# Optimization experiments

Hardware: AMD Instinct MI355X
Metric: run time of the kernel (lower is better)

## Reference

```python
import jax, jax.numpy as jnp
import numpy as np

N = 10000          # in_size: number of nodes
H = 8              # n_heads
D = 64             # dimension per head
FEAT = H * D       # 512, node feature width (heads concatenated)
N_NETS = 3         # number of input networks (modalities)
E = 160000         # edges per network


def setup_inputs() -> dict:
    key = jax.random.key(0)
    ks = jax.random.split(key, 6)
    x = jax.random.normal(ks[0], (N, FEAT), dtype=jnp.float32)
    # n_id: global node ids in the sampled data_flow (here: full graph, identity)
    n_id = jnp.arange(N, dtype=jnp.int32)
    # per-network GAT attention values (non-negative, like softmaxed attn)
    attns = jax.random.uniform(ks[1], (N_NETS, E, H), dtype=jnp.float32)
    # per-network global edge indices (row 0 = source, row 1 = target)
    edges_global = jax.random.randint(ks[2], (N_NETS, 2, E), 0, N, dtype=jnp.int32)
    # learned per-head, per-network combination weights: net_weights[:, net_idx]
    net_weights = jax.random.uniform(ks[3], (H, N_NETS), dtype=jnp.float32)
    # ComboWGATConv linear: in = dimension*n_heads, out = dimension per head (concat)
    W = jax.random.normal(ks[4], (FEAT, FEAT), dtype=jnp.float32) * 0.02
    bias = jnp.zeros((FEAT,), dtype=jnp.float32)
    return {"x": x, "n_id": n_id, "attns": attns, "edges_global": edges_global,
            "net_weights": net_weights, "W": W, "bias": bias}


def reference(x, n_id, attns, edges_global, net_weights, W, bias):
    n_nodes, feat = x.shape
    n_nets, e, h = attns.shape
    d = feat // h

    # --- multi-network attention combination (aggregat_edge_weights) ---
    # w_cogat_attn[i] = net_weights[:, i] * attns[i]   -> (nets, E, H)
    w_attn = attns * net_weights.T[:, None, :]
    # Sparse add/coalesce across modalities: since the subsequent scatter-sum is
    # linear in edge weights, summing duplicate edges is equivalent to keeping
    # the concatenated (non-coalesced) edge list. nets-major flatten order.
    agg_alpha = w_attn.reshape(n_nets * e, h)                      # (Etot, H)
    agg_edges = edges_global.transpose(1, 0, 2).reshape(2, n_nets * e)  # (2, Etot)

    # --- edge_idx_from_global_to_local: invert n_id lookup ---
    inv = jnp.zeros((N,), dtype=jnp.int32).at[n_id].set(
        jnp.arange(n_nodes, dtype=jnp.int32))
    src = inv[agg_edges[0]]
    dst = inv[agg_edges[1]]

    # --- ComboWGATConv with externally supplied alpha (layer_no == 0) ---
    x_l = x[n_id]                                   # gather subgraph features
    hfeat = (x_l @ W).reshape(n_nodes, h, d)        # per-head transform
    msg = agg_alpha[:, :, None] * hfeat[src]        # (Etot, H, D) gather+weight
    out = jax.ops.segment_sum(msg, dst, num_segments=n_nodes)  # scatter-sum
    out = out.reshape(n_nodes, feat) + bias         # concat heads + bias
    return out
```

## Files before the change

### kernel.cpp

```cpp
#include <hip/hip_runtime.h>

#define NNODES 10000
#define NHEADS 8
#define DHEAD 64
#define FEAT 512
#define NNETS 3
#define EDGES 160000
#define ETOT (NNETS * EDGES)
#define NBUCK 4
#define BUCKSZ 2500
#define NKEY (NNODES * NBUCK)

#define CVTX_BLKS 5000
#define CVTW_BLKS 256
#define HIST_BLKS 1875
#define INV_BLKS 40
#define SCAT_BLKS 1875
#define GEMM_BLKS 316

typedef unsigned short ushort_t;
typedef __bf16 bf16x8 __attribute__((ext_vector_type(8)));
typedef float f32x4 __attribute__((ext_vector_type(4)));
typedef unsigned u32x4 __attribute__((ext_vector_type(4)));

static __device__ __forceinline__ ushort_t f2b(float f) {
    unsigned u = __float_as_uint(f);
    unsigned r = u + 0x7FFF + ((u >> 16) & 1);
    return (ushort_t)(r >> 16);
}

static __device__ __forceinline__ void mfma16(f32x4& d, bf16x8 a, bf16x8 b) {
    asm volatile("v_mfma_f32_16x16x32_bf16 %0, %1, %2, %0" : "+v"(d) : "v"(a), "v"(b));
}

#define GLDS(gp, lp)                                                                     \
    __builtin_amdgcn_global_load_lds((const __attribute__((address_space(1))) void*)(gp), \
                                     (__attribute__((address_space(3))) void*)(lp), 16, 0, 0)

__global__ __launch_bounds__(256) void prep_fused_kernel(
    const float* __restrict__ x, ushort_t* __restrict__ xb, const float* __restrict__ W,
    ushort_t* __restrict__ wbt, const int* __restrict__ edges, int* __restrict__ counts,
    const int* __restrict__ n_id, int* __restrict__ inv) {
    __shared__ float tile[32][33];
    int b = blockIdx.x;
    int t = threadIdx.x;
    if (b < CVTX_BLKS) {
        int i = (b * 256 + t) * 4;
        float4 v = *(const float4*)(x + i);
        ushort4 o;
        o.x = f2b(v.x);
        o.y = f2b(v.y);
        o.z = f2b(v.z);
        o.w = f2b(v.w);
        *(ushort4*)(xb + i) = o;
    } else if (b < CVTX_BLKS + CVTW_BLKS) {
        int bb = b - CVTX_BLKS;
        int n0 = (bb & 15) * 32, k0 = (bb >> 4) * 32;
        int r = t >> 3, c4 = (t & 7) * 4;
        float4 v = *(const float4*)(&W[(size_t)(k0 + r) * FEAT + n0 + c4]);
        tile[r][c4 + 0] = v.x;
        tile[r][c4 + 1] = v.y;
        tile[r][c4 + 2] = v.z;
        tile[r][c4 + 3] = v.w;
        __syncthreads();
        ushort4 o;
        o.x = f2b(tile[c4 + 0][r]);
        o.y = f2b(tile[c4 + 1][r]);
        o.z = f2b(tile[c4 + 2][r]);
        o.w = f2b(tile[c4 + 3][r]);
        int ncol = n0 + r;
        int nperm = (ncol & 63) * 8 + (ncol >> 6);
        *(ushort4*)(&wbt[(size_t)nperm * FEAT + k0 + c4]) = o;
    } else if (b < CVTX_BLKS + CVTW_BLKS + HIST_BLKS) {
        int eid = (b - CVTX_BLKS - CVTW_BLKS) * 256 + t;
        int net = eid / EDGES;
        int e = eid - net * EDGES;
        int srcg = edges[net * (2 * EDGES) + e];
        int dstg = edges[net * (2 * EDGES) + EDGES + e];
        atomicAdd(&counts[dstg * NBUCK + srcg / BUCKSZ], 1);
    } else {
        int i = (b - CVTX_BLKS - CVTW_BLKS - HIST_BLKS) * 256 + t;
        if (i < NNODES) inv[n_id[i]] = i;
    }
}

__global__ __launch_bounds__(1024) void scan_kernel(const int* __restrict__ counts,
                                                    int* __restrict__ offsets) {
    __shared__ int wincl[16];
    int t = threadIdx.x;
    int ln = t & 63;
    int w = t >> 6;
    int4 v[10];
    int mysum = 0;
    if (t < 1000) {
        const int4* cp = (const int4*)(counts + t * 40);
#pragma unroll
        for (int i = 0; i < 10; ++i) {
            v[i] = cp[i];
            mysum += v[i].x + v[i].y + v[i].z + v[i].w;
        }
    }
    int s = mysum;
#pragma unroll
    for (int o = 1; o < 64; o <<= 1) {
        int u = __shfl_up(s, o, 64);
        if (ln >= o) s += u;
    }
    if (ln == 63) wincl[w] = s;
    __syncthreads();
    if (w == 0) {
        int ws = (ln < 16) ? wincl[ln] : 0;
#pragma unroll
        for (int o = 1; o < 16; o <<= 1) {
            int u = __shfl_up(ws, o, 64);
            if (ln >= o) ws += u;
        }
        if (ln < 16) wincl[ln] = ws;
    }
    __syncthreads();
    int base = ((w > 0) ? wincl[w - 1] : 0) + s - mysum;
    if (t < 1000) {
        int running = base;
        int* op = offsets + t * 40;
#pragma unroll
        for (int i = 0; i < 10; ++i) {
            op[i * 4 + 0] = running; running += v[i].x;
            op[i * 4 + 1] = running; running += v[i].y;
            op[i * 4 + 2] = running; running += v[i].z;
            op[i * 4 + 3] = running; running += v[i].w;
        }
        if (t == 999) offsets[NKEY] = running;
    }
}

__global__ __launch_bounds__(256) void gemm_scatter_kernel(
    const ushort_t* __restrict__ xb, const ushort_t* __restrict__ wbt,
    ushort_t* __restrict__ Cq, const int* __restrict__ edges,
    const int* __restrict__ inv, const int* __restrict__ offsets,
    int* __restrict__ cursor, const float* __restrict__ attns,
    const float* __restrict__ nw, unsigned* __restrict__ rec) {
    const int t = threadIdx.x;
    if (blockIdx.x < SCAT_BLKS) {
        int eid = blockIdx.x * 256 + t;
        int net = eid / EDGES;
        int e = eid - net * EDGES;
        int srcg = edges[net * (2 * EDGES) + e];
        int dstg = edges[net * (2 * EDGES) + EDGES + e];
        int key = dstg * NBUCK + srcg / BUCKSZ;
        int pos = offsets[key] + atomicAdd(&cursor[key], 1);
        float4 A0 = *(const float4*)(&attns[(size_t)eid * NHEADS]);
        float4 A1 = *(const float4*)(&attns[(size_t)eid * NHEADS + 4]);
        u32x4 w0, w1;
        w0.x = (unsigned)(inv[srcg] << 10);
        w0.y = 0; w0.z = 0; w0.w = 0;
        w1.x = (unsigned)f2b(A0.x * nw[0 * NNETS + net]) |
               ((unsigned)f2b(A0.y * nw[1 * NNETS + net]) << 16);
        w1.y = (unsigned)f2b(A0.z * nw[2 * NNETS + net]) |
               ((unsigned)f2b(A0.w * nw[3 * NNETS + net]) << 16);
        w1.z = (unsigned)f2b(A1.x * nw[4 * NNETS + net]) |
               ((unsigned)f2b(A1.y * nw[5 * NNETS + net]) << 16);
        w1.w = (unsigned)f2b(A1.z * nw[6 * NNETS + net]) |
               ((unsigned)f2b(A1.w * nw[7 * NNETS + net]) << 16);
        *(u32x4*)(&rec[(size_t)pos * 8]) = w0;
        *(u32x4*)(&rec[(size_t)pos * 8 + 4]) = w1;
        return;
    }
    __shared__ ushort_t Alds[128 * 32];
    __shared__ ushort_t Blds[128 * 32];
    const int gb = blockIdx.x - SCAT_BLKS;
    const int wv = t >> 6;
    const int l = t & 63;
    const int lane15 = l & 15;
    const int hi = l >> 4;
    const int r0 = (gb >> 2) * 128;
    const int c0 = (gb & 3) * 128;
    const int WR = (wv >> 1) * 64;
    const int WC = (wv & 1) * 64;

    const int srow = (wv << 4) + (l >> 2);
    const int scol = (l & 3) << 3;
    const ushort_t* Ab0 = xb + (size_t)min(r0 + srow, NNODES - 1) * FEAT + scol;
    const ushort_t* Ab1 = xb + (size_t)min(r0 + 64 + srow, NNODES - 1) * FEAT + scol;
    const ushort_t* Bb0 = wbt + (size_t)(c0 + srow) * FEAT + scol;
    const ushort_t* Bb1 = wbt + (size_t)(c0 + 64 + srow) * FEAT + scol;
    ushort_t* Al0 = &Alds[wv * 512];
    ushort_t* Al1 = &Alds[2048 + wv * 512];
    ushort_t* Bl0 = &Blds[wv * 512];
    ushort_t* Bl1 = &Blds[2048 + wv * 512];

    f32x4 acc[4][4] = {};

    for (int k0 = 0; k0 < FEAT; k0 += 32) {
        GLDS(Ab0 + k0, Al0);
        GLDS(Ab1 + k0, Al1);
        GLDS(Bb0 + k0, Bl0);
        GLDS(Bb1 + k0, Bl1);
        __syncthreads();
        bf16x8 a[4], b[4];
        const ushort_t* Ap = &Alds[(WR + lane15) * 32 + hi * 8];
        const ushort_t* Bp = &Blds[(WC + lane15) * 32 + hi * 8];
#pragma unroll
        for (int m = 0; m < 4; ++m) a[m] = *(const bf16x8*)(Ap + m * 512);
#pragma unroll
        for (int n = 0; n < 4; ++n) b[n] = *(const bf16x8*)(Bp + n * 512);
#pragma unroll
        for (int m = 0; m < 4; ++m)
#pragma unroll
            for (int n = 0; n < 4; ++n) mfma16(acc[m][n], a[m], b[n]);
        __syncthreads();
    }
    asm volatile("s_nop 7\n\ts_nop 7\n\ts_nop 7" ::);
#pragma unroll
    for (int m = 0; m < 4; ++m) {
#pragma unroll
        for (int rr = 0; rr < 4; ++rr) {
            int row = r0 + WR + m * 16 + hi * 4 + rr;
            if (row < NNODES) {
#pragma unroll
                for (int n = 0; n < 4; ++n) {
                    int col = c0 + WC + n * 16 + lane15;
                    Cq[(size_t)row * FEAT + col] = f2b(acc[m][n][rr]);
                }
            }
        }
    }
}

static __device__ __forceinline__ void fma_pair(unsigned a, unsigned h, float& lo,
                                                float& hi) {
    float alo = __uint_as_float(a << 16);
    float ahi = __uint_as_float(a & 0xFFFF0000u);
    float hlo = __uint_as_float(h << 16);
    float hhi = __uint_as_float(h & 0xFFFF0000u);
    lo = fmaf(alo, hlo, lo);
    hi = fmaf(ahi, hhi, hi);
}

__global__ __launch_bounds__(256) void aggregate_kernel(
    const unsigned* __restrict__ rec, const int* __restrict__ offsets,
    const int* __restrict__ n_id, const ushort_t* __restrict__ hfeatq,
    const float* __restrict__ bias, float* __restrict__ out) {
    int wv = threadIdx.x >> 6;
    int d = threadIdx.x & 63;
    const char* hb = (const char*)hfeatq + d * 16;
    int n = blockIdx.x * 4 + wv;
    int g = n_id[n];
    int beg = offsets[g * NBUCK], end = offsets[g * NBUCK + NBUCK];
    float acc[8] = {};
    int k = beg;
    for (; k + 8 <= end; k += 8) {
        unsigned so[8];
#pragma unroll
        for (int i = 0; i < 8; ++i) so[i] = rec[(size_t)(k + i) * 8];
        u32x4 gg[8], aa[8];
#pragma unroll
        for (int i = 0; i < 8; ++i) gg[i] = *(const u32x4*)(hb + so[i]);
#pragma unroll
        for (int i = 0; i < 8; ++i) aa[i] = *(const u32x4*)(&rec[(size_t)(k + i) * 8 + 4]);
#pragma unroll
        for (int i = 0; i < 8; ++i) {
            fma_pair(aa[i].x, gg[i].x, acc[0], acc[1]);
            fma_pair(aa[i].y, gg[i].y, acc[2], acc[3]);
            fma_pair(aa[i].z, gg[i].z, acc[4], acc[5]);
            fma_pair(aa[i].w, gg[i].w, acc[6], acc[7]);
        }
    }
    for (; k < end; ++k) {
        unsigned so = rec[(size_t)k * 8];
        u32x4 a0 = *(const u32x4*)(&rec[(size_t)k * 8 + 4]);
        u32x4 g0 = *(const u32x4*)(hb + so);
        fma_pair(a0.x, g0.x, acc[0], acc[1]);
        fma_pair(a0.y, g0.y, acc[2], acc[3]);
        fma_pair(a0.z, g0.z, acc[4], acc[5]);
        fma_pair(a0.w, g0.w, acc[6], acc[7]);
    }
#pragma unroll
    for (int h = 0; h < NHEADS; ++h) {
        int c = h * DHEAD + d;
        __builtin_nontemporal_store(acc[h] + bias[c], &out[(size_t)n * FEAT + c]);
    }
}

extern "C" void kernel_launch(void* const* d_in, const int* in_sizes, int n_in,
                              void* d_out, int out_size, void* d_ws, size_t ws_size,
                              hipStream_t stream) {
    const float* x = (const float*)d_in[0];
    const int* n_id = (const int*)d_in[1];
    const float* attns = (const float*)d_in[2];
    const int* edges = (const int*)d_in[3];
    const float* nw = (const float*)d_in[4];
    const float* W = (const float*)d_in[5];
    const float* bias = (const float*)d_in[6];
    float* out = (float*)d_out;

    char* ws = (char*)d_ws;
    size_t o = 0;
    ushort_t* hfeatq = (ushort_t*)(ws + o); o += 10240000;
    unsigned* rec    = (unsigned*)(ws + o); o += 15360000;
    ushort_t* xb     = (ushort_t*)(ws + o); o += 10240000;
    ushort_t* wbt    = (ushort_t*)(ws + o); o += 524288;
    int* counts      = (int*)(ws + o);      o += 160000;
    int* cursor      = (int*)(ws + o);      o += 160000;
    int* offsets     = (int*)(ws + o);      o += 160004;
    int* inv         = (int*)(ws + o);      o += 40000;

    hipMemsetAsync(counts, 0, 320000, stream);
    prep_fused_kernel<<<CVTX_BLKS + CVTW_BLKS + HIST_BLKS + INV_BLKS, 256, 0, stream>>>(
        x, xb, W, wbt, edges, counts, n_id, inv);
    scan_kernel<<<1, 1024, 0, stream>>>(counts, offsets);
    gemm_scatter_kernel<<<SCAT_BLKS + GEMM_BLKS, 256, 0, stream>>>(
        xb, wbt, hfeatq, edges, inv, offsets, cursor, attns, nw, rec);
    aggregate_kernel<<<NNODES / 4, 256, 0, stream>>>(rec, offsets, n_id, hfeatq,
                                                     bias, out);
}
```

Baseline: 131.4 us.

## Overlap offset scan with GEMM and split scatter into its own kernel

Moves the prefix scan of the bucket counts out of its own single-block launch and runs it as one extra 256-thread block inside the GEMM kernel. The GEMM no longer waits on the scan, and the edge scatter, which needs the offsets, becomes a separate kernel launched afterwards. Separately, the aggregate kernel gets an occupancy hint of 8 blocks per CU and its gather loop unroll drops from 8 to 4 to lower register pressure. The trade-off is that the scan now uses 256 threads, each doing a longer serial loop, and scatter can no longer overlap with the GEMM.

```diff
diff --git a/kernel.cpp b/kernel.cpp
--- a/kernel.cpp
+++ b/kernel.cpp
@@ -84,20 +84,20 @@
     }
 }
 
-__global__ __launch_bounds__(1024) void scan_kernel(const int* __restrict__ counts,
-                                                    int* __restrict__ offsets) {
-    __shared__ int wincl[16];
+static __device__ void scan_block256(const int* __restrict__ counts,
+                                     int* __restrict__ offsets) {
+    __shared__ int wsum[4];
     int t = threadIdx.x;
-    int ln = t & 63;
-    int w = t >> 6;
-    int4 v[10];
+    int ln = t & 63, w = t >> 6;
+    const int PER = 160;
+    int lo = t * PER;
     int mysum = 0;
-    if (t < 1000) {
-        const int4* cp = (const int4*)(counts + t * 40);
-#pragma unroll
-        for (int i = 0; i < 10; ++i) {
-            v[i] = cp[i];
-            mysum += v[i].x + v[i].y + v[i].z + v[i].w;
+    if (lo < NKEY) {
+        const int4* cp = (const int4*)(counts + lo);
+#pragma unroll 4
+        for (int i = 0; i < 40; ++i) {
+            int4 c = cp[i];
+            mysum += c.x + c.y + c.z + c.w;
         }
     }
     int s = mysum;
@@ -106,68 +106,41 @@
         int u = __shfl_up(s, o, 64);
         if (ln >= o) s += u;
     }
-    if (ln == 63) wincl[w] = s;
+    if (ln == 63) wsum[w] = s;
     __syncthreads();
-    if (w == 0) {
-        int ws = (ln < 16) ? wincl[ln] : 0;
-#pragma unroll
-        for (int o = 1; o < 16; o <<= 1) {
-            int u = __shfl_up(ws, o, 64);
-            if (ln >= o) ws += u;
+    int base = s - mysum;
+    for (int i = 0; i < w; ++i) base += wsum[i];
+    if (lo < NKEY) {
+        int running = base;
+        const int4* cp = (const int4*)(counts + lo);
+        int4* op = (int4*)(offsets + lo);
+#pragma unroll 4
+        for (int i = 0; i < 40; ++i) {
+            int4 c = cp[i];
+            int4 o4;
+            o4.x = running; running += c.x;
+            o4.y = running; running += c.y;
+            o4.z = running; running += c.z;
+            o4.w = running; running += c.w;
+            op[i] = o4;
         }
-        if (ln < 16) wincl[ln] = ws;
-    }
-    __syncthreads();
-    int base = ((w > 0) ? wincl[w - 1] : 0) + s - mysum;
-    if (t < 1000) {
-        int running = base;
-        int* op = offsets + t * 40;
-#pragma unroll
-        for (int i = 0; i < 10; ++i) {
-            op[i * 4 + 0] = running; running += v[i].x;
-            op[i * 4 + 1] = running; running += v[i].y;
-            op[i * 4 + 2] = running; running += v[i].z;
-            op[i * 4 + 3] = running; running += v[i].w;
-        }
-        if (t == 999) offsets[NKEY] = running;
-    }
-}
-
-__global__ __launch_bounds__(256) void gemm_scatter_kernel(
-    const ushort_t* __restrict__ xb, const ushort_t* __restrict__ wbt,
-    ushort_t* __restrict__ Cq, const int* __restrict__ edges,
-    const int* __restrict__ inv, const int* __restrict__ offsets,
-    int* __restrict__ cursor, const float* __restrict__ attns,
-    const float* __restrict__ nw, unsigned* __restrict__ rec) {
+        if (lo + PER == NKEY) offsets[NKEY] = running;
+    }
+}
+
+__global__ __launch_bounds__(256) void scan_gemm_kernel(const ushort_t* __restrict__ xb,
+                                                        const ushort_t* __restrict__ wbt,
+                                                        ushort_t* __restrict__ Cq,
+                                                        const int* __restrict__ counts,
+                                                        int* __restrict__ offsets) {
     const int t = threadIdx.x;
-    if (blockIdx.x < SCAT_BLKS) {
-        int eid = blockIdx.x * 256 + t;
-        int net = eid / EDGES;
-        int e = eid - net * EDGES;
-        int srcg = edges[net * (2 * EDGES) + e];
-        int dstg = edges[net * (2 * EDGES) + EDGES + e];
-        int key = dstg * NBUCK + srcg / BUCKSZ;
-        int pos = offsets[key] + atomicAdd(&cursor[key], 1);
-        float4 A0 = *(const float4*)(&attns[(size_t)eid * NHEADS]);
-        float4 A1 = *(const float4*)(&attns[(size_t)eid * NHEADS + 4]);
-        u32x4 w0, w1;
-        w0.x = (unsigned)(inv[srcg] << 10);
-        w0.y = 0; w0.z = 0; w0.w = 0;
-        w1.x = (unsigned)f2b(A0.x * nw[0 * NNETS + net]) |
-               ((unsigned)f2b(A0.y * nw[1 * NNETS + net]) << 16);
-        w1.y = (unsigned)f2b(A0.z * nw[2 * NNETS + net]) |
-               ((unsigned)f2b(A0.w * nw[3 * NNETS + net]) << 16);
-        w1.z = (unsigned)f2b(A1.x * nw[4 * NNETS + net]) |
-               ((unsigned)f2b(A1.y * nw[5 * NNETS + net]) << 16);
-        w1.w = (unsigned)f2b(A1.z * nw[6 * NNETS + net]) |
-               ((unsigned)f2b(A1.w * nw[7 * NNETS + net]) << 16);
-        *(u32x4*)(&rec[(size_t)pos * 8]) = w0;
-        *(u32x4*)(&rec[(size_t)pos * 8 + 4]) = w1;
+    if (blockIdx.x >= GEMM_BLKS) {
+        scan_block256(counts, offsets);
         return;
     }
     __shared__ ushort_t Alds[128 * 32];
     __shared__ ushort_t Blds[128 * 32];
-    const int gb = blockIdx.x - SCAT_BLKS;
+    const int gb = blockIdx.x;
     const int wv = t >> 6;
     const int l = t & 63;
     const int lane15 = l & 15;
@@ -226,6 +199,37 @@
     }
 }
 
+__global__ __launch_bounds__(256) void scatter_kernel(const int* __restrict__ edges,
+                                                      const int* __restrict__ inv,
+                                                      const int* __restrict__ offsets,
+                                                      int* __restrict__ cursor,
+                                                      const float* __restrict__ attns,
+                                                      const float* __restrict__ nw,
+                                                      unsigned* __restrict__ rec) {
+    int eid = blockIdx.x * 256 + threadIdx.x;
+    int net = eid / EDGES;
+    int e = eid - net * EDGES;
+    int srcg = edges[net * (2 * EDGES) + e];
+    int dstg = edges[net * (2 * EDGES) + EDGES + e];
+    int key = dstg * NBUCK + srcg / BUCKSZ;
+    int pos = offsets[key] + atomicAdd(&cursor[key], 1);
+    float4 A0 = *(const float4*)(&attns[(size_t)eid * NHEADS]);
+    float4 A1 = *(const float4*)(&attns[(size_t)eid * NHEADS + 4]);
+    u32x4 w0, w1;
+    w0.x = (unsigned)(inv[srcg] << 10);
+    w0.y = 0; w0.z = 0; w0.w = 0;
+    w1.x = (unsigned)f2b(A0.x * nw[0 * NNETS + net]) |
+           ((unsigned)f2b(A0.y * nw[1 * NNETS + net]) << 16);
+    w1.y = (unsigned)f2b(A0.z * nw[2 * NNETS + net]) |
+           ((unsigned)f2b(A0.w * nw[3 * NNETS + net]) << 16);
+    w1.z = (unsigned)f2b(A1.x * nw[4 * NNETS + net]) |
+           ((unsigned)f2b(A1.y * nw[5 * NNETS + net]) << 16);
+    w1.w = (unsigned)f2b(A1.z * nw[6 * NNETS + net]) |
+           ((unsigned)f2b(A1.w * nw[7 * NNETS + net]) << 16);
+    *(u32x4*)(&rec[(size_t)pos * 8]) = w0;
+    *(u32x4*)(&rec[(size_t)pos * 8 + 4]) = w1;
+}
+
 static __device__ __forceinline__ void fma_pair(unsigned a, unsigned h, float& lo,
                                                 float& hi) {
     float alo = __uint_as_float(a << 16);
@@ -236,7 +240,7 @@
     hi = fmaf(ahi, hhi, hi);
 }
 
-__global__ __launch_bounds__(256) void aggregate_kernel(
+__global__ __launch_bounds__(256, 8) void aggregate_kernel(
     const unsigned* __restrict__ rec, const int* __restrict__ offsets,
     const int* __restrict__ n_id, const ushort_t* __restrict__ hfeatq,
     const float* __restrict__ bias, float* __restrict__ out) {
@@ -248,22 +252,35 @@
     int beg = offsets[g * NBUCK], end = offsets[g * NBUCK + NBUCK];
     float acc[8] = {};
     int k = beg;
-    for (; k + 8 <= end; k += 8) {
-        unsigned so[8];
-#pragma unroll
-        for (int i = 0; i < 8; ++i) so[i] = rec[(size_t)(k + i) * 8];
-        u32x4 gg[8], aa[8];
-#pragma unroll
-        for (int i = 0; i < 8; ++i) gg[i] = *(const u32x4*)(hb + so[i]);
-#pragma unroll
-        for (int i = 0; i < 8; ++i) aa[i] = *(const u32x4*)(&rec[(size_t)(k + i) * 8 + 4]);
-#pragma unroll
-        for (int i = 0; i < 8; ++i) {
-            fma_pair(aa[i].x, gg[i].x, acc[0], acc[1]);
-            fma_pair(aa[i].y, gg[i].y, acc[2], acc[3]);
-            fma_pair(aa[i].z, gg[i].z, acc[4], acc[5]);
-            fma_pair(aa[i].w, gg[i].w, acc[6], acc[7]);
-        }
+    for (; k + 4 <= end; k += 4) {
+        unsigned so0 = rec[(size_t)(k + 0) * 8];
+        unsigned so1 = rec[(size_t)(k + 1) * 8];
+        unsigned so2 = rec[(size_t)(k + 2) * 8];
+        unsigned so3 = rec[(size_t)(k + 3) * 8];
+        u32x4 g0 = *(const u32x4*)(hb + so0);
+        u32x4 g1 = *(const u32x4*)(hb + so1);
+        u32x4 g2 = *(const u32x4*)(hb + so2);
+        u32x4 g3 = *(const u32x4*)(hb + so3);
+        u32x4 a0 = *(const u32x4*)(&rec[(size_t)(k + 0) * 8 + 4]);
+        u32x4 a1 = *(const u32x4*)(&rec[(size_t)(k + 1) * 8 + 4]);
+        u32x4 a2 = *(const u32x4*)(&rec[(size_t)(k + 2) * 8 + 4]);
+        u32x4 a3 = *(const u32x4*)(&rec[(size_t)(k + 3) * 8 + 4]);
+        fma_pair(a0.x, g0.x, acc[0], acc[1]);
+        fma_pair(a0.y, g0.y, acc[2], acc[3]);
+        fma_pair(a0.z, g0.z, acc[4], acc[5]);
+        fma_pair(a0.w, g0.w, acc[6], acc[7]);
+        fma_pair(a1.x, g1.x, acc[0], acc[1]);
+        fma_pair(a1.y, g1.y, acc[2], acc[3]);
+        fma_pair(a1.z, g1.z, acc[4], acc[5]);
+        fma_pair(a1.w, g1.w, acc[6], acc[7]);
+        fma_pair(a2.x, g2.x, acc[0], acc[1]);
+        fma_pair(a2.y, g2.y, acc[2], acc[3]);
+        fma_pair(a2.z, g2.z, acc[4], acc[5]);
+        fma_pair(a2.w, g2.w, acc[6], acc[7]);
+        fma_pair(a3.x, g3.x, acc[0], acc[1]);
+        fma_pair(a3.y, g3.y, acc[2], acc[3]);
+        fma_pair(a3.z, g3.z, acc[4], acc[5]);
+        fma_pair(a3.w, g3.w, acc[6], acc[7]);
     }
     for (; k < end; ++k) {
         unsigned so = rec[(size_t)k * 8];
@@ -307,9 +324,9 @@
     hipMemsetAsync(counts, 0, 320000, stream);
     prep_fused_kernel<<<CVTX_BLKS + CVTW_BLKS + HIST_BLKS + INV_BLKS, 256, 0, stream>>>(
         x, xb, W, wbt, edges, counts, n_id, inv);
-    scan_kernel<<<1, 1024, 0, stream>>>(counts, offsets);
-    gemm_scatter_kernel<<<SCAT_BLKS + GEMM_BLKS, 256, 0, stream>>>(
-        xb, wbt, hfeatq, edges, inv, offsets, cursor, attns, nw, rec);
+    scan_gemm_kernel<<<GEMM_BLKS + 1, 256, 0, stream>>>(xb, wbt, hfeatq, counts, offsets);
+    scatter_kernel<<<SCAT_BLKS, 256, 0, stream>>>(edges, inv, offsets, cursor, attns, nw,
+                                                  rec);
     aggregate_kernel<<<NNODES / 4, 256, 0, stream>>>(rec, offsets, n_id, hfeatq,
                                                      bias, out);
 }
```

Result: no change. 133.9 us (+1.9%).
